# Kernel tuning notes

Hardware: AMD Instinct MI355X
Metric: run time of the kernel (lower is better)

The kernel has to match this reference:

```python
import jax, jax.numpy as jnp
import numpy as np

B, L, D, V, C = 128, 128, 512, 50000, 512  # batch, leaves, embed_dim, vocab, num_category
NODES = 2 * L - 1


def setup_inputs() -> dict:
    key = jax.random.key(0)
    k1, k2, k3, k4 = jax.random.split(key, 4)
    leaf_content_id = jax.random.randint(k1, (B, L), 0, V)
    # leaves occupy positions 0..L-1; internal nodes fill L..2L-2 during compose
    content_mask = jnp.concatenate(
        [jnp.ones((B, L), dtype=bool), jnp.zeros((B, L - 1), dtype=bool)], axis=1)
    # each step composes two already-available nodes; leaf indices are always valid
    composition_info = jax.random.randint(k2, (B, L - 1, 2), 0, L)
    emb_weight = jax.random.normal(k3, (V, D), dtype=jnp.float32) * 0.02
    lin_w = jax.random.normal(k4, (C, D), dtype=jnp.float32) * 0.02
    lin_b = jnp.zeros((C,), dtype=jnp.float32)
    return dict(leaf_content_id=leaf_content_id, content_mask=content_mask,
                composition_info=composition_info, emb_weight=emb_weight,
                lin_w=lin_w, lin_b=lin_b)


def circular_correlation(a, b):
    # corr(a, b) = irfft(conj(rfft(a)) * rfft(b))
    fa = jnp.fft.rfft(a, axis=-1)
    fb = jnp.fft.rfft(b, axis=-1)
    return jnp.fft.irfft(jnp.conj(fa) * fb, n=a.shape[-1], axis=-1)


def reference(leaf_content_id, content_mask, composition_info, emb_weight, lin_w, lin_b):
    Bq, Lq = leaf_content_id.shape
    nodes = 2 * Lq - 1
    Dq = emb_weight.shape[1]
    # embed leaves into positions where content_mask is True (first L slots)
    leaf_vec = emb_weight[leaf_content_id]                      # [B, L, D]
    vector = jnp.zeros((Bq, nodes, Dq), dtype=emb_weight.dtype)
    vector = vector.at[:, :Lq].set(jnp.where(content_mask[:, :Lq, None], leaf_vec, 0.0))
    batch_ar = jnp.arange(Bq)

    def step(vec, xs):
        idx, li, ri = xs                                        # li, ri: [B]
        left = vec[batch_ar, li]                                # gather [B, D]
        right = vec[batch_ar, ri]
        comp = circular_correlation(left, right)                # [B, D]
        # internal node for step idx lands at position L + idx (rolled mask)
        vec = jax.lax.dynamic_update_slice(vec, comp[:, None, :], (0, Lq + idx, 0))
        return vec, None

    xs = (jnp.arange(Lq - 1),
          composition_info[:, :, 0].T.astype(jnp.int32),
          composition_info[:, :, 1].T.astype(jnp.int32))
    vector, _ = jax.lax.scan(step, vector, xs)
    logits = jnp.einsum('bnd,cd->bnc', vector, lin_w) + lin_b   # [B, 2L-1, C]
    return jax.nn.sigmoid(logits)
```

## Files before the change

### kernel.cpp

```cpp
#include <hip/hip_runtime.h>
#include <hip/hip_bf16.h>

#define Bq 128
#define Lq 128
#define Dq 512
#define NODES 255
#define Cq 512
#define M_ROWS (Bq * NODES)
#define FP8_SCALE 64.0f
#define INV_SCALE2 (1.0f / (FP8_SCALE * FP8_SCALE))

typedef unsigned int uint32;
typedef unsigned char uchar;
typedef _Float16 v8hf __attribute__((ext_vector_type(8)));
typedef __fp16 v2fp __attribute__((ext_vector_type(2)));
typedef float v4f __attribute__((ext_vector_type(4)));
typedef unsigned int v4u __attribute__((ext_vector_type(4)));

__device__ inline uint32 packh(float lo, float hi) {
    v2fp p = __builtin_amdgcn_cvt_pkrtz(lo, hi);
    return __builtin_bit_cast(uint32, p);
}
__device__ inline uint32 fp8x4(float a, float b, float c, float d) {
    int lo = __builtin_amdgcn_cvt_pk_fp8_f32(a, b, 0, false);
    return (uint32)__builtin_amdgcn_cvt_pk_fp8_f32(c, d, lo, true);
}
__device__ inline uchar fp8b(float a) {
    return (uchar)(__builtin_amdgcn_cvt_pk_fp8_f32(a, a, 0, false) & 0xFF);
}

__global__ __launch_bounds__(256) void wconv_kernel(const float* __restrict__ linw,
                                                    uchar* __restrict__ wb) {
    int i = (blockIdx.x * 256 + threadIdx.x) * 8;
    float4 v0 = *((const float4*)(linw + i));
    float4 v1 = *((const float4*)(linw + i + 4));
    uint2 o;
    o.x = fp8x4(v0.x * FP8_SCALE, v0.y * FP8_SCALE, v0.z * FP8_SCALE, v0.w * FP8_SCALE);
    o.y = fp8x4(v1.x * FP8_SCALE, v1.y * FP8_SCALE, v1.z * FP8_SCALE, v1.w * FP8_SCALE);
    *((uint2*)(wb + i)) = o;
}

#define CW2 1040

__global__ __launch_bounds__(512, 4) void fused_kernel(const int* __restrict__ ids,
                                                       const int* __restrict__ cinfo,
                                                       const float* __restrict__ emb,
                                                       const uchar* __restrict__ wb,
                                                       const float* __restrict__ bias,
                                                       float* __restrict__ out) {
    __shared__ __align__(16) uchar smem[32768 + CW2 * 4 * 8];
    uchar* Vt = smem;
    uint32* scratch = (uint32*)(smem + 32768);
    int t = threadIdx.x;
    int wave = t >> 6, lane = t & 63;
    int blk = blockIdx.x;

    uint32* W = scratch + wave * CW2;
    int q = lane >> 4, m = lane & 15;

    int aid[8], cid[8];
#pragma unroll
    for (int ri = 0; ri < 8; ++ri) {
        int r = ri * 8 + wave;
        if (ri < 4) {
            int lidx = blk * 32 + r;
            int b = lidx >> 7, node = lidx & 127;
            aid[ri] = ids[b * Lq + node];
            cid[ri] = -1;
        } else {
            int iidx = blk * 32 + r - 32;
            if (iidx > 16255) iidx = 16255;
            int b = iidx / 127, idx = iidx - b * 127;
            int li = cinfo[(b * 127 + idx) * 2 + 0];
            int rx = cinfo[(b * 127 + idx) * 2 + 1];
            aid[ri] = ids[b * Lq + li];
            cid[ri] = ids[b * Lq + rx];
        }
    }

#pragma unroll
    for (int ri = 0; ri < 8; ++ri) {
        int r = ri * 8 + wave;
        int key = (r & 7) << 4;
        uchar* vrow = Vt + r * 512;
        const float4* ar = (const float4*)(emb + (size_t)aid[ri] * Dq);
        float4 a0 = ar[2 * lane], a1 = ar[2 * lane + 1];
        if (ri < 4) {
            uint2 o;
            o.x = fp8x4(a0.x * FP8_SCALE, a0.y * FP8_SCALE, a0.z * FP8_SCALE, a0.w * FP8_SCALE);
            o.y = fp8x4(a1.x * FP8_SCALE, a1.y * FP8_SCALE, a1.z * FP8_SCALE, a1.w * FP8_SCALE);
            int byte = (((lane >> 1) << 4) ^ key) | ((lane & 1) << 3);
            *((uint2*)(vrow + byte)) = o;
        } else {
            const float4* cr = (const float4*)(emb + (size_t)cid[ri] * Dq);
            float4 c0 = cr[2 * lane], c1 = cr[2 * lane + 1];
            v4u ua = {packh(a0.x, a0.y), packh(a0.z, a0.w), packh(a1.x, a1.y), packh(a1.z, a1.w)};
            v4u ub = {packh(c0.x, c0.y), packh(c0.z, c0.w), packh(c1.x, c1.y), packh(c1.z, c1.w)};
            ((v4u*)(W))[lane] = ua;
            ((v4u*)(W + 256))[lane] = ua;
            ((v4u*)(W + 512))[lane] = ub;
            if (lane < 2) ((v4u*)(W + 768))[lane] = ub;
            uint32 dn = (uint32)__shfl((int)ub.x, (lane + 1) & 63);
            v4u uo;
            uo.x = __builtin_amdgcn_alignbit(ub.y, ub.x, 16);
            uo.y = __builtin_amdgcn_alignbit(ub.z, ub.y, 16);
            uo.z = __builtin_amdgcn_alignbit(ub.w, ub.z, 16);
            uo.w = __builtin_amdgcn_alignbit(dn,   ub.w, 16);
            ((v4u*)(W + 776))[lane] = uo;
            if (lane < 2) ((v4u*)(W + 1032))[lane] = uo;

            const uint32* A0 = W + (4 * q - 8 * m + 256);
            const uint32* A1 = W + (4 * q - 8 * m + 128);
            const uint32* PB = W + ((lane & 1) ? 776 : 512) + 4 * q + (m >> 1);
            v4f acc0 = {0.f, 0.f, 0.f, 0.f};
            v4f acc1 = {0.f, 0.f, 0.f, 0.f};
#pragma unroll
            for (int kb = 0; kb < 16; ++kb) {
                v4u Ra = *((const v4u*)(A0 + 16 * kb));
                v4u Rb = *((const v4u*)(A1 + 16 * kb));
                v4u RB;
                RB.x = PB[16 * kb + 0]; RB.y = PB[16 * kb + 1];
                RB.z = PB[16 * kb + 2]; RB.w = PB[16 * kb + 3];
                v8hf fa0 = __builtin_bit_cast(v8hf, Ra);
                v8hf fa1 = __builtin_bit_cast(v8hf, Rb);
                v8hf fb  = __builtin_bit_cast(v8hf, RB);
                acc0 = __builtin_amdgcn_mfma_f32_16x16x32_f16(fa0, fb, acc0, 0, 0, 0);
                acc1 = __builtin_amdgcn_mfma_f32_16x16x32_f16(fa1, fb, acc1, 0, 0, 0);
            }
#pragma unroll
            for (int rr2 = 0; rr2 < 4; ++rr2) {
                int ch = 4 * q + rr2;
                vrow[(((ch)      << 4) ^ key) | m] = fp8b(acc0[rr2] * FP8_SCALE);
                vrow[(((ch + 16) << 4) ^ key) | m] = fp8b(acc1[rr2] * FP8_SCALE);
            }
        }
    }

    int quad = lane >> 4, qq = lane & 15;
    int qhi = quad >> 1, qlo = quad & 1;
    int cw = wave * 64;

    const uchar* wp[4];
#pragma unroll
    for (int i = 0; i < 4; ++i)
        wp[i] = wb + (size_t)(cw + 16 * i + qq) * Dq + 8 * quad;
    long wreg[4];
#pragma unroll
    for (int i = 0; i < 4; ++i)
        wreg[i] = *((const long*)(wp[i]));

    __syncthreads();

    v4f acc[4][4];
#pragma unroll
    for (int i = 0; i < 4; ++i)
#pragma unroll
        for (int j = 0; j < 4; ++j)
            acc[i][j] = (v4f){0.f, 0.f, 0.f, 0.f};

#pragma unroll
    for (int ks = 0; ks < 16; ++ks) {
        long wcur[4];
#pragma unroll
        for (int i = 0; i < 4; ++i) wcur[i] = wreg[i];
        if (ks < 15) {
#pragma unroll
            for (int i = 0; i < 4; ++i)
                wreg[i] = *((const long*)(wp[i] + 32 * (ks + 1)));
        }
        long vf[4];
#pragma unroll
        for (int j = 0; j < 4; ++j) {
            int row = 16 * j + qq;
            int phys = (2 * ks + qhi) ^ (qq & 7);
            vf[j] = *((const long*)(Vt + row * 512 + phys * 16 + qlo * 8));
        }
#pragma unroll
        for (int i = 0; i < 4; ++i)
#pragma unroll
            for (int j = 0; j < 4; ++j)
                acc[i][j] = __builtin_amdgcn_mfma_f32_16x16x32_fp8_fp8(wcur[i], vf[j], acc[i][j], 0, 0, 0);
    }

#pragma unroll
    for (int i = 0; i < 4; ++i) {
        int cb = cw + 16 * i + 4 * quad;
        float4 b4 = *((const float4*)(bias + cb));
#pragma unroll
        for (int j = 0; j < 4; ++j) {
            int r = 16 * j + qq;
            int grow;
            if (j < 2) {
                int lidx = blk * 32 + r;
                grow = (lidx >> 7) * 255 + (lidx & 127);
            } else {
                int iidx = blk * 32 + r - 32;
                if (iidx > 16255) iidx = 16255;
                int bb = iidx / 127;
                grow = bb * 255 + 128 + (iidx - bb * 127);
            }
            float4 o4;
            o4.x = 1.f / (1.f + __expf(-(acc[i][j][0] * INV_SCALE2 + b4.x)));
            o4.y = 1.f / (1.f + __expf(-(acc[i][j][1] * INV_SCALE2 + b4.y)));
            o4.z = 1.f / (1.f + __expf(-(acc[i][j][2] * INV_SCALE2 + b4.z)));
            o4.w = 1.f / (1.f + __expf(-(acc[i][j][3] * INV_SCALE2 + b4.w)));
            *((float4*)(out + (size_t)grow * Cq + cb)) = o4;
        }
    }
}

extern "C" void kernel_launch(void* const* d_in, const int* in_sizes, int n_in,
                              void* d_out, int out_size, void* d_ws, size_t ws_size,
                              hipStream_t stream) {
    const int*   ids   = (const int*)d_in[0];
    const int*   cinfo = (const int*)d_in[2];
    const float* emb   = (const float*)d_in[3];
    const float* linw  = (const float*)d_in[4];
    const float* linb  = (const float*)d_in[5];
    float* out = (float*)d_out;

    uchar* wb = (uchar*)d_ws;

    wconv_kernel<<<dim3(128), dim3(256), 0, stream>>>(linw, wb);
    fused_kernel<<<dim3(512), dim3(512), 0, stream>>>(ids, cinfo, emb, wb, linb, out);

    (void)in_sizes; (void)n_in; (void)out_size; (void)ws_size;
}
```

Before: 204.9 us.

## Prefetch embedding rows ahead and double-buffer weight fragments in GEMM loop

```diff
diff --git a/kernel.cpp b/kernel.cpp
--- a/kernel.cpp
+++ b/kernel.cpp
@@ -78,61 +78,88 @@
         }
     }
 
-#pragma unroll
-    for (int ri = 0; ri < 8; ++ri) {
+    float4 la[4][2];
+#pragma unroll
+    for (int ri = 0; ri < 4; ++ri) {
+        const float4* ar = (const float4*)(emb + (size_t)aid[ri] * Dq);
+        la[ri][0] = ar[2 * lane];
+        la[ri][1] = ar[2 * lane + 1];
+    }
+    float4 na0, na1, nc0, nc1;
+    {
+        const float4* ar = (const float4*)(emb + (size_t)aid[4] * Dq);
+        const float4* cr = (const float4*)(emb + (size_t)cid[4] * Dq);
+        na0 = ar[2 * lane]; na1 = ar[2 * lane + 1];
+        nc0 = cr[2 * lane]; nc1 = cr[2 * lane + 1];
+    }
+    __builtin_amdgcn_sched_barrier(0);
+
+#pragma unroll
+    for (int ri = 0; ri < 4; ++ri) {
         int r = ri * 8 + wave;
         int key = (r & 7) << 4;
         uchar* vrow = Vt + r * 512;
-        const float4* ar = (const float4*)(emb + (size_t)aid[ri] * Dq);
-        float4 a0 = ar[2 * lane], a1 = ar[2 * lane + 1];
-        if (ri < 4) {
-            uint2 o;
-            o.x = fp8x4(a0.x * FP8_SCALE, a0.y * FP8_SCALE, a0.z * FP8_SCALE, a0.w * FP8_SCALE);
-            o.y = fp8x4(a1.x * FP8_SCALE, a1.y * FP8_SCALE, a1.z * FP8_SCALE, a1.w * FP8_SCALE);
-            int byte = (((lane >> 1) << 4) ^ key) | ((lane & 1) << 3);
-            *((uint2*)(vrow + byte)) = o;
-        } else {
-            const float4* cr = (const float4*)(emb + (size_t)cid[ri] * Dq);
-            float4 c0 = cr[2 * lane], c1 = cr[2 * lane + 1];
-            v4u ua = {packh(a0.x, a0.y), packh(a0.z, a0.w), packh(a1.x, a1.y), packh(a1.z, a1.w)};
-            v4u ub = {packh(c0.x, c0.y), packh(c0.z, c0.w), packh(c1.x, c1.y), packh(c1.z, c1.w)};
-            ((v4u*)(W))[lane] = ua;
-            ((v4u*)(W + 256))[lane] = ua;
-            ((v4u*)(W + 512))[lane] = ub;
-            if (lane < 2) ((v4u*)(W + 768))[lane] = ub;
-            uint32 dn = (uint32)__shfl((int)ub.x, (lane + 1) & 63);
-            v4u uo;
-            uo.x = __builtin_amdgcn_alignbit(ub.y, ub.x, 16);
-            uo.y = __builtin_amdgcn_alignbit(ub.z, ub.y, 16);
-            uo.z = __builtin_amdgcn_alignbit(ub.w, ub.z, 16);
-            uo.w = __builtin_amdgcn_alignbit(dn,   ub.w, 16);
-            ((v4u*)(W + 776))[lane] = uo;
-            if (lane < 2) ((v4u*)(W + 1032))[lane] = uo;
-
-            const uint32* A0 = W + (4 * q - 8 * m + 256);
-            const uint32* A1 = W + (4 * q - 8 * m + 128);
-            const uint32* PB = W + ((lane & 1) ? 776 : 512) + 4 * q + (m >> 1);
-            v4f acc0 = {0.f, 0.f, 0.f, 0.f};
-            v4f acc1 = {0.f, 0.f, 0.f, 0.f};
-#pragma unroll
-            for (int kb = 0; kb < 16; ++kb) {
-                v4u Ra = *((const v4u*)(A0 + 16 * kb));
-                v4u Rb = *((const v4u*)(A1 + 16 * kb));
-                v4u RB;
-                RB.x = PB[16 * kb + 0]; RB.y = PB[16 * kb + 1];
-                RB.z = PB[16 * kb + 2]; RB.w = PB[16 * kb + 3];
-                v8hf fa0 = __builtin_bit_cast(v8hf, Ra);
-                v8hf fa1 = __builtin_bit_cast(v8hf, Rb);
-                v8hf fb  = __builtin_bit_cast(v8hf, RB);
-                acc0 = __builtin_amdgcn_mfma_f32_16x16x32_f16(fa0, fb, acc0, 0, 0, 0);
-                acc1 = __builtin_amdgcn_mfma_f32_16x16x32_f16(fa1, fb, acc1, 0, 0, 0);
-            }
-#pragma unroll
-            for (int rr2 = 0; rr2 < 4; ++rr2) {
-                int ch = 4 * q + rr2;
-                vrow[(((ch)      << 4) ^ key) | m] = fp8b(acc0[rr2] * FP8_SCALE);
-                vrow[(((ch + 16) << 4) ^ key) | m] = fp8b(acc1[rr2] * FP8_SCALE);
-            }
+        uint2 o;
+        o.x = fp8x4(la[ri][0].x * FP8_SCALE, la[ri][0].y * FP8_SCALE,
+                    la[ri][0].z * FP8_SCALE, la[ri][0].w * FP8_SCALE);
+        o.y = fp8x4(la[ri][1].x * FP8_SCALE, la[ri][1].y * FP8_SCALE,
+                    la[ri][1].z * FP8_SCALE, la[ri][1].w * FP8_SCALE);
+        int byte = (((lane >> 1) << 4) ^ key) | ((lane & 1) << 3);
+        *((uint2*)(vrow + byte)) = o;
+    }
+
+#pragma unroll
+    for (int ri = 4; ri < 8; ++ri) {
+        float4 a0 = na0, a1 = na1, c0 = nc0, c1 = nc1;
+        if (ri < 7) {
+            const float4* ar = (const float4*)(emb + (size_t)aid[ri + 1] * Dq);
+            const float4* cr = (const float4*)(emb + (size_t)cid[ri + 1] * Dq);
+            na0 = ar[2 * lane]; na1 = ar[2 * lane + 1];
+            nc0 = cr[2 * lane]; nc1 = cr[2 * lane + 1];
+        }
+        __builtin_amdgcn_sched_barrier(0);
+
+        int r = ri * 8 + wave;
+        int key = (r & 7) << 4;
+        uchar* vrow = Vt + r * 512;
+        v4u ua = {packh(a0.x, a0.y), packh(a0.z, a0.w), packh(a1.x, a1.y), packh(a1.z, a1.w)};
+        v4u ub = {packh(c0.x, c0.y), packh(c0.z, c0.w), packh(c1.x, c1.y), packh(c1.z, c1.w)};
+        ((v4u*)(W))[lane] = ua;
+        ((v4u*)(W + 256))[lane] = ua;
+        ((v4u*)(W + 512))[lane] = ub;
+        if (lane < 2) ((v4u*)(W + 768))[lane] = ub;
+        uint32 dn = (uint32)__shfl((int)ub.x, (lane + 1) & 63);
+        v4u uo;
+        uo.x = __builtin_amdgcn_alignbit(ub.y, ub.x, 16);
+        uo.y = __builtin_amdgcn_alignbit(ub.z, ub.y, 16);
+        uo.z = __builtin_amdgcn_alignbit(ub.w, ub.z, 16);
+        uo.w = __builtin_amdgcn_alignbit(dn,   ub.w, 16);
+        ((v4u*)(W + 776))[lane] = uo;
+        if (lane < 2) ((v4u*)(W + 1032))[lane] = uo;
+
+        const uint32* A0 = W + (4 * q - 8 * m + 256);
+        const uint32* A1 = W + (4 * q - 8 * m + 128);
+        const uint32* PB = W + ((lane & 1) ? 776 : 512) + 4 * q + (m >> 1);
+        v4f acc0 = {0.f, 0.f, 0.f, 0.f};
+        v4f acc1 = {0.f, 0.f, 0.f, 0.f};
+#pragma unroll
+        for (int kb = 0; kb < 16; ++kb) {
+            v4u Ra = *((const v4u*)(A0 + 16 * kb));
+            v4u Rb = *((const v4u*)(A1 + 16 * kb));
+            v4u RB;
+            RB.x = PB[16 * kb + 0]; RB.y = PB[16 * kb + 1];
+            RB.z = PB[16 * kb + 2]; RB.w = PB[16 * kb + 3];
+            v8hf fa0 = __builtin_bit_cast(v8hf, Ra);
+            v8hf fa1 = __builtin_bit_cast(v8hf, Rb);
+            v8hf fb  = __builtin_bit_cast(v8hf, RB);
+            acc0 = __builtin_amdgcn_mfma_f32_16x16x32_f16(fa0, fb, acc0, 0, 0, 0);
+            acc1 = __builtin_amdgcn_mfma_f32_16x16x32_f16(fa1, fb, acc1, 0, 0, 0);
+        }
+#pragma unroll
+        for (int rr2 = 0; rr2 < 4; ++rr2) {
+            int ch = 4 * q + rr2;
+            vrow[(((ch)      << 4) ^ key) | m] = fp8b(acc0[rr2] * FP8_SCALE);
+            vrow[(((ch + 16) << 4) ^ key) | m] = fp8b(acc1[rr2] * FP8_SCALE);
         }
     }
 
@@ -144,10 +171,12 @@
 #pragma unroll
     for (int i = 0; i < 4; ++i)
         wp[i] = wb + (size_t)(cw + 16 * i + qq) * Dq + 8 * quad;
-    long wreg[4];
-#pragma unroll
-    for (int i = 0; i < 4; ++i)
-        wreg[i] = *((const long*)(wp[i]));
+    long wregA[4], wregB[4];
+#pragma unroll
+    for (int i = 0; i < 4; ++i) {
+        wregA[i] = *((const long*)(wp[i]));
+        wregB[i] = *((const long*)(wp[i] + 32));
+    }
 
     __syncthreads();
 
@@ -162,11 +191,14 @@
     for (int ks = 0; ks < 16; ++ks) {
         long wcur[4];
 #pragma unroll
-        for (int i = 0; i < 4; ++i) wcur[i] = wreg[i];
-        if (ks < 15) {
+        for (int i = 0; i < 4; ++i) {
+            wcur[i] = wregA[i];
+            wregA[i] = wregB[i];
+        }
+        if (ks < 14) {
 #pragma unroll
             for (int i = 0; i < 4; ++i)
-                wreg[i] = *((const long*)(wp[i] + 32 * (ks + 1)));
+                wregB[i] = *((const long*)(wp[i] + 32 * (ks + 2)));
         }
         long vf[4];
 #pragma unroll
```

New measurement: 200.8 us. 2.0% less time.
